# Optimization experiments

Hardware: AMD Instinct MI355X
Metric: run time of the kernel (lower is better)

## Reference

```python
import jax, jax.numpy as jnp
import numpy as np

N_NODES = 10000
N_EDGES = 160000
C = 16        # num_feature_channels
C2 = 8        # output channels per irrep per head (C/2)
HID = 64      # radial_network_hidden_units
NH = 2        # num_attention_heads
NG = 16       # graphs in batch
F_IN = 64     # num_features
F_OUT = 32    # number_of_output_features
HEAD_TYPES = ("normal", "inverse")  # invariant_dictionary
IRREP_SLICES = ((0, 1), (1, 4), (4, 9))  # l=0,1,2 blocks of the SH dim


def _sph_harm(r):
    """Component-normalized real spherical harmonics l=0..2 for unit vectors r [E,3] -> [E,9]."""
    x, y, z = r[:, 0], r[:, 1], r[:, 2]
    c3 = 1.7320508   # sqrt(3)
    c15 = 3.8729833  # sqrt(15)
    l0 = jnp.ones_like(x)[:, None]
    l1 = c3 * r
    l2 = jnp.stack([
        c15 * x * y,
        c15 * y * z,
        1.1180340 * (2.0 * z * z - x * x - y * y),  # sqrt(5)/2
        c15 * x * z,
        1.9364917 * (x * x - y * y),                 # sqrt(15)/2
    ], axis=-1)
    return jnp.concatenate([l0, l1, l2], axis=-1)


def setup_inputs() -> dict:
    key = jax.random.key(0)
    ks = jax.random.split(key, 16)
    node_features = jax.random.normal(ks[0], (N_NODES, F_IN), jnp.float32)
    pos = jax.random.normal(ks[1], (N_NODES, 3), jnp.float32)
    src = jax.random.randint(ks[2], (N_EDGES,), 0, N_NODES)
    off = jax.random.randint(ks[3], (N_EDGES,), 1, N_NODES)  # avoid self-loops (d=0)
    tgt = (src + off) % N_NODES
    edge_index = jnp.stack([src, tgt], axis=0)
    batch = jnp.sort(jax.random.randint(ks[4], (N_NODES,), 0, NG))
    s = lambda k, shape, fan: (jax.random.normal(k, shape, jnp.float32) / np.sqrt(fan)).astype(jnp.float32)
    return dict(
        node_features=node_features, pos=pos,
        W_embed=s(ks[5], (F_IN, C), F_IN), b_embed=jnp.zeros((C,), jnp.float32),
        Wq=s(ks[6], (NH, C, C), C), Wk=s(ks[7], (NH, C, C), C),
        W1=s(ks[8], (NH, 1, HID), 1), b1=jnp.zeros((NH, HID), jnp.float32),
        Wa=s(ks[9], (NH, HID), HID), Wv=s(ks[10], (NH, HID, C * 3), HID),
        Wo=s(ks[11], (NH, 3, C, C2), C),
        Wproj=s(ks[12], (NH * C2, F_OUT), NH * C2), bproj=jnp.zeros((F_OUT,), jnp.float32),
        edge_index=edge_index, batch=batch,
    )


def _forward(node_features, pos, W_embed, b_embed, Wq, Wk, W1, b1, Wa, Wv, Wo,
             Wproj, bproj, edge_index, batch):
    src, tgt = edge_index[0], edge_index[1]
    rel = pos[tgt] - pos[src]                       # [E,3]
    dist = jnp.linalg.norm(rel, axis=-1, keepdims=True)  # [E,1]
    rhat = rel / dist
    Y = _sph_harm(rhat)                             # [E,9]
    x = node_features @ W_embed + b_embed          # [N,C] scalar (0e) features
    xs = x[src]                                     # [E,C]
    inv_sqrt_c = 1.0 / np.sqrt(C)
    head_outs = []
    for h in range(NH):
        d_feat = dist if HEAD_TYPES[h] == "normal" else dist ** -2  # [E,1]
        hid = jax.nn.relu(d_feat @ W1[h] + b1[h])   # [E,HID] radial network
        att_bias = hid @ Wa[h]                      # [E]
        wv = (hid @ Wv[h]).reshape(-1, C, 3)        # [E,C,3] per-(channel,l) radial weights
        q = x @ Wq[h]
        k = x @ Wk[h]
        logit = jnp.sum(q[tgt] * k[src], axis=-1) * inv_sqrt_c + att_bias  # [E]
        # segment softmax over incoming edges of each target node
        m = jax.ops.segment_max(logit, tgt, num_segments=N_NODES)
        e = jnp.exp(logit - m[tgt])
        z = jax.ops.segment_sum(e, tgt, num_segments=N_NODES)
        alpha = e / z[tgt]                          # [E]
        # expand per-l weights to per-m: dims (1,3,5)
        wv_m = jnp.repeat(wv, np.array([1, 3, 5]), axis=2, total_repeat_length=9)  # [E,C,9]
        msg = (alpha[:, None, None] * wv_m) * xs[:, :, None] * Y[:, None, :]       # [E,C,9]
        node_out = jax.ops.segment_sum(msg, tgt, num_segments=N_NODES)             # [N,C,9]
        parts = [jnp.einsum('ncm,co->nom', node_out[:, :, s0:s1], Wo[h, li]).reshape(N_NODES, -1)
                 for li, (s0, s1) in enumerate(IRREP_SLICES)]
        head_outs.append(jnp.concatenate(parts, axis=-1))  # [N, C2*9]
    feat = jnp.concatenate(head_outs, axis=-1)              # [N, NH*C2*9]
    pooled = jax.ops.segment_sum(feat, batch, num_segments=NG)  # [NG, NH*C2*9]
    # equivariant Linear -> F_OUT x 0e: only scalar (l=0) components map to scalars
    blk = C2 * 9
    scal = jnp.concatenate([pooled[:, h * blk: h * blk + C2] for h in range(NH)], axis=-1)  # [NG, NH*C2]
    return scal @ Wproj + bproj                             # [NG, F_OUT]


def reference(node_features, pos, W_embed, b_embed, Wq, Wk, W1, b1, Wa, Wv, Wo,
              Wproj, bproj, edge_index, batch):
    return _forward(node_features, pos, W_embed, b_embed, Wq, Wk, W1, b1, Wa, Wv,
                    Wo, Wproj, bproj, edge_index, batch)
```

## Files before the change

kernel.cpp:

```cpp
#include <hip/hip_runtime.h>
#include <math.h>

#define NN 10000
#define NE 160000
#define CAP 96

__global__ __launch_bounds__(256) void k_xqk(const float* __restrict__ nf,
        const float* __restrict__ We, const float* __restrict__ be,
        const float* __restrict__ Wq, const float* __restrict__ Wk,
        const float* __restrict__ Wv,
        float* __restrict__ x, float* __restrict__ q, float* __restrict__ k,
        int* __restrict__ zeroReg, float* __restrict__ vC) {
    int t = threadIdx.x;
    int gid = blockIdx.x * 256 + t;
    if (gid < 10256) zeroReg[gid] = 0;
    if (blockIdx.x == 0) {
        for (int i = t; i < 2048; i += 256) {
            int h = i >> 10, j = (i >> 4) & 63, c = i & 15;
            vC[i] = Wv[(h * 64 + j) * 48 + 3 * c];
        }
    }
    __shared__ float sWe[64 * 16];
    __shared__ float sWq[2 * 16 * 16];
    __shared__ float sWk[2 * 16 * 16];
    __shared__ float sNF[16 * 64];
    __shared__ float sX[16 * 16];
    for (int i = t; i < 1024; i += 256) sWe[i] = We[i];
    for (int i = t; i < 512; i += 256) { sWq[i] = Wq[i]; sWk[i] = Wk[i]; }
    int nodeBase = blockIdx.x * 16;
    for (int i = t; i < 1024; i += 256) {
        int n = nodeBase + (i >> 6);
        sNF[i] = (n < NN) ? nf[n * 64 + (i & 63)] : 0.0f;
    }
    __syncthreads();
    int ln = t >> 4, c = t & 15;
    int n = nodeBase + ln;
    float acc = be[c];
    #pragma unroll 16
    for (int j = 0; j < 64; ++j) acc = fmaf(sNF[ln * 64 + j], sWe[j * 16 + c], acc);
    sX[ln * 16 + c] = acc;
    __syncthreads();
    if (n < NN) {
        x[n * 16 + c] = acc;
        #pragma unroll
        for (int h = 0; h < 2; ++h) {
            float aq = 0.0f, ak = 0.0f;
            #pragma unroll
            for (int j = 0; j < 16; ++j) {
                float xv = sX[ln * 16 + j];
                aq = fmaf(xv, sWq[(h * 16 + j) * 16 + c], aq);
                ak = fmaf(xv, sWk[(h * 16 + j) * 16 + c], ak);
            }
            q[(n * 2 + h) * 16 + c] = aq;
            k[(n * 2 + h) * 16 + c] = ak;
        }
    }
}

__global__ __launch_bounds__(256) void k_edge(const float* __restrict__ pos,
        const int* __restrict__ ei,
        const float* __restrict__ q, const float* __restrict__ k,
        const float* __restrict__ W1, const float* __restrict__ b1,
        const float* __restrict__ Wa, const float* __restrict__ vC,
        const float* __restrict__ Wo,
        const float* __restrict__ x, int* __restrict__ deg,
        float* __restrict__ lgp, float* __restrict__ gws) {
    int e = blockIdx.x * 256 + threadIdx.x;
    if (e >= NE) return;
    int s = ei[e], t = ei[NE + e];
    int p = atomicAdd(&deg[t], 1);
    bool ok = (p < CAP);
    size_t slot = (size_t)t * CAP + p;
    float dx = pos[t * 3 + 0] - pos[s * 3 + 0];
    float dy = pos[t * 3 + 1] - pos[s * 3 + 1];
    float dz = pos[t * 3 + 2] - pos[s * 3 + 2];
    float d = sqrtf(dx * dx + dy * dy + dz * dz);
    float fh[2] = { d, 1.0f / (d * d) };
    const float4* xp = (const float4*)(x + (size_t)s * 16);
    float4 xs0 = xp[0], xs1 = xp[1], xs2 = xp[2], xs3 = xp[3];
    float xf[16] = { xs0.x, xs0.y, xs0.z, xs0.w, xs1.x, xs1.y, xs1.z, xs1.w,
                     xs2.x, xs2.y, xs2.z, xs2.w, xs3.x, xs3.y, xs3.z, xs3.w };
    float L2v[2];
    #pragma unroll
    for (int h = 0; h < 2; ++h) {
        const float4* qt = (const float4*)(q + (size_t)t * 32 + h * 16);
        const float4* ks = (const float4*)(k + (size_t)s * 32 + h * 16);
        float4 a0 = qt[0], a1 = qt[1], a2 = qt[2], a3 = qt[3];
        float4 b0 = ks[0], c1 = ks[1], c2 = ks[2], c3 = ks[3];
        float dot = a0.x * b0.x + a0.y * b0.y + a0.z * b0.z + a0.w * b0.w
                  + a1.x * c1.x + a1.y * c1.y + a1.z * c1.z + a1.w * c1.w
                  + a2.x * c2.x + a2.y * c2.y + a2.z * c2.z + a2.w * c2.w
                  + a3.x * c3.x + a3.y * c3.y + a3.z * c3.z + a3.w * c3.w;
        float f = fh[h];
        float att = 0.0f;
        float acc[16];
        #pragma unroll
        for (int c = 0; c < 16; ++c) acc[c] = 0.0f;
        const float* w1b = W1 + h * 64;
        const float* b1b = b1 + h * 64;
        const float* wab = Wa + h * 64;
        const float* vcb = vC + h * 1024;
        #pragma unroll 8
        for (int j = 0; j < 64; ++j) {
            float hid = fmaxf(fmaf(f, w1b[j], b1b[j]), 0.0f);
            att = fmaf(hid, wab[j], att);
            #pragma unroll
            for (int c = 0; c < 16; ++c)
                acc[c] = fmaf(hid, vcb[j * 16 + c], acc[c]);
        }
        L2v[h] = fmaf(dot, 0.25f, att);
        float g[8];
        #pragma unroll
        for (int o = 0; o < 8; ++o) g[o] = 0.0f;
        const float* wob = Wo + h * 384;
        #pragma unroll
        for (int c = 0; c < 16; ++c) {
            float axc = acc[c] * xf[c];
            #pragma unroll
            for (int o = 0; o < 8; ++o) g[o] = fmaf(axc, wob[c * 8 + o], g[o]);
        }
        if (ok) {
            float4* gp = (float4*)(gws + slot * 16 + h * 8);
            gp[0] = make_float4(g[0], g[1], g[2], g[3]);
            gp[1] = make_float4(g[4], g[5], g[6], g[7]);
        }
    }
    if (ok) *(float2*)(lgp + slot * 2) = make_float2(L2v[0], L2v[1]);
}

__global__ __launch_bounds__(256) void k_gather(const int* __restrict__ deg,
        const float* __restrict__ lgp, const float* __restrict__ gws,
        float* __restrict__ feat) {
    int t0 = threadIdx.x;
    int wv = t0 >> 6;
    int lane = t0 & 63;
    int pid = blockIdx.x * 4 + wv;
    int n = pid >> 1, h = pid & 1;
    int dg = min(deg[n], CAP);
    int g = lane >> 3, o = lane & 7;
    float m = -INFINITY, z = 0.0f, u = 0.0f;
    const float* lgb = lgp + (size_t)n * (CAP * 2) + h;
    const float* gwb = gws + (size_t)n * (CAP * 16) + h * 8 + o;
    for (int i = g; i < dg; i += 8) {
        float L  = lgb[i * 2];
        float gv = gwb[(size_t)i * 16];
        float nm = fmaxf(m, L);
        float sc = (m > -INFINITY) ? __expf(m - nm) : 0.0f;
        float w  = __expf(L - nm);
        u = fmaf(u, sc, w * gv);
        z = fmaf(z, sc, w);
        m = nm;
    }
    #pragma unroll
    for (int off = 8; off <= 32; off <<= 1) {
        float mo = __shfl_xor(m, off, 64);
        float zo = __shfl_xor(z, off, 64);
        float uo = __shfl_xor(u, off, 64);
        float nm = fmaxf(m, mo);
        float a = (m  > -INFINITY) ? __expf(m  - nm) : 0.0f;
        float b = (mo > -INFINITY) ? __expf(mo - nm) : 0.0f;
        u = u * a + uo * b;
        z = z * a + zo * b;
        m = nm;
    }
    float un = (z > 0.0f) ? u / z : 0.0f;
    if (lane < 8) feat[n * 16 + h * 8 + o] = un;
}

__global__ __launch_bounds__(256) void k_pool(const float* __restrict__ feat,
        const int* __restrict__ batch, float* __restrict__ pooled) {
    __shared__ float sP[256];
    int t = threadIdx.x;
    sP[t] = 0.0f;
    __syncthreads();
    for (int i = blockIdx.x * 256 + t; i < NN * 16; i += 40 * 256) {
        int n = i >> 4, c = i & 15;
        atomicAdd(&sP[batch[n] * 16 + c], feat[i]);
    }
    __syncthreads();
    atomicAdd(&pooled[t], sP[t]);
}

__global__ __launch_bounds__(512) void k_final(const float* __restrict__ pooled,
        const float* __restrict__ Wproj, const float* __restrict__ bproj,
        float* __restrict__ out) {
    int t = threadIdx.x;
    int g = t >> 5, fo = t & 31;
    float acc = bproj[fo];
    #pragma unroll
    for (int j = 0; j < 16; ++j) acc = fmaf(pooled[g * 16 + j], Wproj[j * 32 + fo], acc);
    out[g * 32 + fo] = acc;
}

extern "C" void kernel_launch(void* const* d_in, const int* in_sizes, int n_in,
                              void* d_out, int out_size, void* d_ws, size_t ws_size,
                              hipStream_t stream) {
    const float* nf    = (const float*)d_in[0];
    const float* pos   = (const float*)d_in[1];
    const float* We    = (const float*)d_in[2];
    const float* be    = (const float*)d_in[3];
    const float* Wq    = (const float*)d_in[4];
    const float* Wk    = (const float*)d_in[5];
    const float* W1    = (const float*)d_in[6];
    const float* b1    = (const float*)d_in[7];
    const float* Wa    = (const float*)d_in[8];
    const float* Wv    = (const float*)d_in[9];
    const float* Wo    = (const float*)d_in[10];
    const float* Wproj = (const float*)d_in[11];
    const float* bproj = (const float*)d_in[12];
    const int*   ei    = (const int*)d_in[13];
    const int*   batch = (const int*)d_in[14];
    float* out = (float*)d_out;
    (void)in_sizes; (void)n_in; (void)out_size; (void)ws_size;

    float* ws     = (float*)d_ws;
    float* x      = ws;
    float* q      = x + 160000;
    float* k      = q + 320000;
    float* feat   = k + 320000;
    float* pooled = feat + 160000;
    int*   deg    = (int*)(pooled + 256);
    float* vC     = (float*)(deg + 10000);
    float* lgp    = vC + 2048;
    float* gws    = lgp + (size_t)NN * CAP * 2;

    hipLaunchKernelGGL(k_xqk,    dim3(625),  dim3(256), 0, stream, nf, We, be, Wq, Wk, Wv, x, q, k, (int*)pooled, vC);
    hipLaunchKernelGGL(k_edge,   dim3(625),  dim3(256), 0, stream, pos, ei, q, k, W1, b1, Wa, vC, Wo, x, deg, lgp, gws);
    hipLaunchKernelGGL(k_gather, dim3(5000), dim3(256), 0, stream, deg, lgp, gws, feat);
    hipLaunchKernelGGL(k_pool,   dim3(40),   dim3(256), 0, stream, feat, batch, pooled);
    hipLaunchKernelGGL(k_final,  dim3(1),    dim3(512), 0, stream, pooled, Wproj, bproj, out);
}
```

Measured before the change: 133.0 us.

## Store per-edge messages as bf16 and pool features with per-thread run sums

Per-edge projected messages are packed to bf16 pairs, halving the bytes k_edge writes and k_gather reads. The gather now has each lane handle two channels over 16 edge groups instead of one channel over 8. k_pool is rewritten so each thread sums a contiguous run of 16 nodes per channel and issues one shared atomic per graph change, rather than one atomic per element. Rounding messages to bf16 lowers precision of the softmax-weighted sums.

After: 130.0 us. 1.02x faster.

```diff
diff --git a/kernel.cpp b/kernel.cpp
--- a/kernel.cpp
+++ b/kernel.cpp
@@ -4,6 +4,14 @@
 #define NN 10000
 #define NE 160000
 #define CAP 96
+
+__device__ __forceinline__ unsigned bf16pack2(float a, float b) {
+    unsigned ua = __float_as_uint(a);
+    unsigned ub = __float_as_uint(b);
+    ua = ua + 0x7fffu + ((ua >> 16) & 1u);
+    ub = ub + 0x7fffu + ((ub >> 16) & 1u);
+    return (ua >> 16) | (ub & 0xffff0000u);
+}
 
 __global__ __launch_bounds__(256) void k_xqk(const float* __restrict__ nf,
         const float* __restrict__ We, const float* __restrict__ be,
@@ -64,7 +72,7 @@
         const float* __restrict__ Wa, const float* __restrict__ vC,
         const float* __restrict__ Wo,
         const float* __restrict__ x, int* __restrict__ deg,
-        float* __restrict__ lgp, float* __restrict__ gws) {
+        float* __restrict__ lgp, uint4* __restrict__ gb) {
     int e = blockIdx.x * 256 + threadIdx.x;
     if (e >= NE) return;
     int s = ei[e], t = ei[NE + e];
@@ -120,16 +128,15 @@
             for (int o = 0; o < 8; ++o) g[o] = fmaf(axc, wob[c * 8 + o], g[o]);
         }
         if (ok) {
-            float4* gp = (float4*)(gws + slot * 16 + h * 8);
-            gp[0] = make_float4(g[0], g[1], g[2], g[3]);
-            gp[1] = make_float4(g[4], g[5], g[6], g[7]);
+            gb[slot * 2 + h] = make_uint4(bf16pack2(g[0], g[1]), bf16pack2(g[2], g[3]),
+                                          bf16pack2(g[4], g[5]), bf16pack2(g[6], g[7]));
         }
     }
     if (ok) *(float2*)(lgp + slot * 2) = make_float2(L2v[0], L2v[1]);
 }
 
 __global__ __launch_bounds__(256) void k_gather(const int* __restrict__ deg,
-        const float* __restrict__ lgp, const float* __restrict__ gws,
+        const float* __restrict__ lgp, const unsigned* __restrict__ gb,
         float* __restrict__ feat) {
     int t0 = threadIdx.x;
     int wv = t0 >> 6;
@@ -137,34 +144,41 @@
     int pid = blockIdx.x * 4 + wv;
     int n = pid >> 1, h = pid & 1;
     int dg = min(deg[n], CAP);
-    int g = lane >> 3, o = lane & 7;
-    float m = -INFINITY, z = 0.0f, u = 0.0f;
+    int g = lane >> 2, p = lane & 3;
+    float m = -INFINITY, z = 0.0f, u0 = 0.0f, u1 = 0.0f;
     const float* lgb = lgp + (size_t)n * (CAP * 2) + h;
-    const float* gwb = gws + (size_t)n * (CAP * 16) + h * 8 + o;
-    for (int i = g; i < dg; i += 8) {
-        float L  = lgb[i * 2];
-        float gv = gwb[(size_t)i * 16];
+    const unsigned* gbb = gb + (size_t)n * (CAP * 8) + h * 4 + p;
+    for (int i = g; i < dg; i += 16) {
+        float L = lgb[i * 2];
+        unsigned wbits = gbb[(size_t)i * 8];
+        float ga = __uint_as_float(wbits << 16);
+        float gbv = __uint_as_float(wbits & 0xffff0000u);
         float nm = fmaxf(m, L);
         float sc = (m > -INFINITY) ? __expf(m - nm) : 0.0f;
         float w  = __expf(L - nm);
-        u = fmaf(u, sc, w * gv);
-        z = fmaf(z, sc, w);
+        u0 = fmaf(u0, sc, w * ga);
+        u1 = fmaf(u1, sc, w * gbv);
+        z  = fmaf(z, sc, w);
         m = nm;
     }
     #pragma unroll
-    for (int off = 8; off <= 32; off <<= 1) {
+    for (int off = 4; off <= 32; off <<= 1) {
         float mo = __shfl_xor(m, off, 64);
         float zo = __shfl_xor(z, off, 64);
-        float uo = __shfl_xor(u, off, 64);
+        float a0o = __shfl_xor(u0, off, 64);
+        float a1o = __shfl_xor(u1, off, 64);
         float nm = fmaxf(m, mo);
         float a = (m  > -INFINITY) ? __expf(m  - nm) : 0.0f;
         float b = (mo > -INFINITY) ? __expf(mo - nm) : 0.0f;
-        u = u * a + uo * b;
-        z = z * a + zo * b;
+        u0 = u0 * a + a0o * b;
+        u1 = u1 * a + a1o * b;
+        z  = z * a + zo * b;
         m = nm;
     }
-    float un = (z > 0.0f) ? u / z : 0.0f;
-    if (lane < 8) feat[n * 16 + h * 8 + o] = un;
+    if (lane < 4) {
+        float inv = (z > 0.0f) ? 1.0f / z : 0.0f;
+        *(float2*)(feat + n * 16 + h * 8 + p * 2) = make_float2(u0 * inv, u1 * inv);
+    }
 }
 
 __global__ __launch_bounds__(256) void k_pool(const float* __restrict__ feat,
@@ -173,10 +187,20 @@
     int t = threadIdx.x;
     sP[t] = 0.0f;
     __syncthreads();
-    for (int i = blockIdx.x * 256 + t; i < NN * 16; i += 40 * 256) {
-        int n = i >> 4, c = i & 15;
-        atomicAdd(&sP[batch[n] * 16 + c], feat[i]);
-    }
+    int tid = blockIdx.x * 256 + t;
+    int c = tid & 15, seg = tid >> 4;
+    int n0 = seg * 16, n1 = min(n0 + 16, NN);
+    float run = 0.0f;
+    int curg = -1;
+    for (int n = n0; n < n1; ++n) {
+        int gg = batch[n];
+        if (gg != curg) {
+            if (curg >= 0) atomicAdd(&sP[curg * 16 + c], run);
+            run = 0.0f; curg = gg;
+        }
+        run += feat[n * 16 + c];
+    }
+    if (curg >= 0) atomicAdd(&sP[curg * 16 + c], run);
     __syncthreads();
     atomicAdd(&pooled[t], sP[t]);
 }
@@ -222,11 +246,11 @@
     int*   deg    = (int*)(pooled + 256);
     float* vC     = (float*)(deg + 10000);
     float* lgp    = vC + 2048;
-    float* gws    = lgp + (size_t)NN * CAP * 2;
+    unsigned* gbu = (unsigned*)(lgp + (size_t)NN * CAP * 2);
 
     hipLaunchKernelGGL(k_xqk,    dim3(625),  dim3(256), 0, stream, nf, We, be, Wq, Wk, Wv, x, q, k, (int*)pooled, vC);
-    hipLaunchKernelGGL(k_edge,   dim3(625),  dim3(256), 0, stream, pos, ei, q, k, W1, b1, Wa, vC, Wo, x, deg, lgp, gws);
-    hipLaunchKernelGGL(k_gather, dim3(5000), dim3(256), 0, stream, deg, lgp, gws, feat);
+    hipLaunchKernelGGL(k_edge,   dim3(625),  dim3(256), 0, stream, pos, ei, q, k, W1, b1, Wa, vC, Wo, x, deg, lgp, (uint4*)gbu);
+    hipLaunchKernelGGL(k_gather, dim3(5000), dim3(256), 0, stream, deg, lgp, gbu, feat);
     hipLaunchKernelGGL(k_pool,   dim3(40),   dim3(256), 0, stream, feat, batch, pooled);
     hipLaunchKernelGGL(k_final,  dim3(1),    dim3(512), 0, stream, pooled, Wproj, bproj, out);
 }
```
